# Performance work log

Hardware: AMD Instinct MI355X
Metric: run time of the kernel (lower is better)

## Reference

```python
import jax, jax.numpy as jnp
import numpy as np

# Module hyperparameters (from init_kwargs)
IOU_T = 0.5
PROB_T = 0.75
COV = 10.0
TOPK = 500       # self.topk
PRE_K = 2048     # fixed-shape cap on post-threshold candidates entering NMS
B, C, H, W = 4, 4, 160, 160


def setup_inputs() -> dict:
    key = jax.random.key(0)
    k1, k2 = jax.random.split(key)
    mask = jax.random.normal(k1, (B, C, H, W), dtype=jnp.float32)
    # scale bias so boxes have ~10px extent (realistic detections)
    bias = jax.random.normal(k2, (B, 4, H, W), dtype=jnp.float32) * 8.0
    return {"mask": mask, "bias": bias}


def _pos_grid(h, w):
    # equivalent of np.dstack(np.mgrid[0:h, 0:w]) -> [h, w, 2] with (y, x)
    yy, xx = jnp.meshgrid(jnp.arange(h), jnp.arange(w), indexing="ij")
    return jnp.stack([yy, xx], axis=-1).astype(jnp.float32)


def _pairwise_iou(b):
    # b: [K, 4] as (y1, x1, y2, x2); torchvision-style IoU (areas unclamped, inter clamped)
    area = (b[:, 2] - b[:, 0]) * (b[:, 3] - b[:, 1])
    lt = jnp.maximum(b[:, None, :2], b[None, :, :2])
    rb = jnp.minimum(b[:, None, 2:], b[None, :, 2:])
    wh = jnp.clip(rb - lt, 0.0)
    inter = wh[..., 0] * wh[..., 1]
    return inter / (area[:, None] + area[None, :] - inter)


def _nms_keep(iou, valid, thresh):
    # boxes are pre-sorted by descending score; greedy suppression
    K = iou.shape[0]
    idx = jnp.arange(K)
    def body(i, keep):
        sup = (iou[i] > thresh) & (idx > i) & keep[i]
        return keep & ~sup
    return jax.lax.fori_loop(0, K, body, valid)


def _per_image(mask_i, bias_i, pos):
    # mask_i: [C, h, w], bias_i: [4, h, w], pos: [h, w, 2]
    p = jax.nn.softmax(mask_i, axis=0)
    prob = jax.lax.stop_gradient(p.max(axis=0))          # prob.detach()
    cls = p.argmax(axis=0)
    frontal = (cls != 0) & (prob > PROB_T)               # [h, w]
    # boxes = pos tiled to (y,x,y,x) + bias.permute(0,2,3,1)
    boxes = jnp.concatenate([pos, pos], axis=-1) + jnp.transpose(bias_i, (1, 2, 0))
    boxes = boxes.reshape(-1, 4)                          # [h*w, 4]
    score = jnp.where(frontal.reshape(-1), prob.reshape(-1), -1.0)
    # fixed-size candidate set, sorted by descending score (invalid -> -1)
    top_s, idx = jax.lax.top_k(score, PRE_K)
    cand = boxes[idx]
    valid = top_s > 0.0                                   # valid scores > PROB_T > 0
    keep = _nms_keep(_pairwise_iou(cand), valid, IOU_T)
    kept_s = jnp.where(keep, top_s, -1.0)
    fin_s, fi = jax.lax.top_k(kept_s, TOPK)               # min(topk, n) via padding
    fboxes = cand[fi]                                     # [TOPK, 4]
    fvalid = fin_s > 0.0
    fprob = jnp.where(fvalid, fin_s, 0.0)
    mu = (fboxes[:, :2] + fboxes[:, 2:]) * 0.5            # [TOPK, 2]
    sigma = fboxes[:, 2:] - fboxes[:, :2]
    sigma = jnp.where(fvalid[:, None], sigma, 1.0)        # safe divisor for padding
    # gaussian2d: z = (pos - mu) / (sigma / cov); heat = max_n exp(-|z|^2/2) * prob
    z = (pos[None] - mu[:, None, None, :]) / (sigma[:, None, None, :] / COV)  # [TOPK,h,w,2]
    g = jnp.exp(-0.5 * (z ** 2).sum(axis=-1)) * fprob[:, None, None]
    heat = g.max(axis=0)                                  # [h, w]; all-padded -> 0, matches n==0 case
    return heat, fboxes, fvalid


def reference(mask, bias):
    pos = _pos_grid(mask.shape[2], mask.shape[3])
    heat, fboxes, fvalid = jax.vmap(lambda m, b: _per_image(m, b, pos))(mask, bias)
    # original returns (heatmaps, mask, boxes); boxes padded to [B, TOPK, 4] with validity mask
    return heat, mask, fboxes, fvalid
```

## Files before the change

kernel.cpp:

```cpp
#include <hip/hip_runtime.h>
#include <math.h>

#define BATCH 4
#define NCH 4
#define H 160
#define W 160
#define NPIX (H * W)
#define NTILE (NPIX / 256)
#define PRE_K 2048
#define TOPK 500
#define PROB_T 0.75f
#define IOU_T 0.5f
#define COV 10.0f

#define SCORE_OFF 0u
#define KEY_OFF   409600u
#define F_OFF     1228800u
#define CSC_OFF   1261632u
#define CBOX_OFF  1294400u
#define SUP_OFF   1425472u
#define NV_OFF    3523648u
#define PAR_OFF   3523712u
#define FLAG_OFF  3563712u
#define BCNT_OFF  3571904u

#define OUT_HEAT_OFF 0
#define OUT_MASK_OFF 102400
#define OUT_BOX_OFF  512000
#define OUT_VAL_OFF  520000

typedef unsigned long long u64;
typedef unsigned int u32;

__device__ __forceinline__ int block_scan_excl(int v, int tid, int* tmp, int* total) {
    tmp[tid] = v;
    __syncthreads();
    for (int off = 1; off < 256; off <<= 1) {
        int y = (tid >= off) ? tmp[tid - off] : 0;
        __syncthreads();
        tmp[tid] += y;
        __syncthreads();
    }
    int incl = tmp[tid];
    *total = tmp[255];
    __syncthreads();
    return incl - v;
}

__global__ void k_score(const float* __restrict__ mask, float* __restrict__ score,
                        float* __restrict__ out_mask, int* __restrict__ blkcnt) {
    int b = blockIdx.y;
    int pix = blockIdx.x * 256 + threadIdx.x;
    const float* mp = mask + (size_t)b * NCH * NPIX + pix;
    float* op = out_mask + (size_t)b * NCH * NPIX + pix;
    float x0 = mp[0], x1 = mp[NPIX], x2 = mp[2 * NPIX], x3 = mp[3 * NPIX];
    op[0] = x0; op[NPIX] = x1; op[2 * NPIX] = x2; op[3 * NPIX] = x3;
    float m = x0; int c = 0;
    if (x1 > m) { m = x1; c = 1; }
    if (x2 > m) { m = x2; c = 2; }
    if (x3 > m) { m = x3; c = 3; }
    float sum = ((expf(x0 - m) + expf(x1 - m)) + expf(x2 - m)) + expf(x3 - m);
    float prob = 1.0f / sum;
    bool frontal = (c != 0) && (prob > PROB_T);
    score[(size_t)b * NPIX + pix] = frontal ? prob : -1.0f;
    __shared__ int wcnt[4];
    u64 bm = __ballot(frontal);
    if ((threadIdx.x & 63) == 0) wcnt[threadIdx.x >> 6] = __popcll(bm);
    __syncthreads();
    if (threadIdx.x == 0)
        blkcnt[b * NTILE + blockIdx.x] = wcnt[0] + wcnt[1] + wcnt[2] + wcnt[3];
}

__global__ void __launch_bounds__(256)
k_compact(const float* __restrict__ score, const float* __restrict__ bias,
          const int* __restrict__ blkcnt, u64* __restrict__ keys,
          int* __restrict__ Fout, float* __restrict__ cand_score,
          float* __restrict__ cand_box) {
    int b = blockIdx.y;
    int bx = blockIdx.x;
    int tid = threadIdx.x;
    const int* bc = blkcnt + b * NTILE;
    int f_base = 0, F = 0;
    #pragma unroll 4
    for (int k = 0; k < NTILE; ++k) {
        int c = bc[k];
        F += c;
        if (k < bx) f_base += c;
    }
    int pix = bx * 256 + tid;
    float s = score[(size_t)b * NPIX + pix];
    bool fr = (s > 0.0f);
    int lane = tid & 63, wv = tid >> 6;
    int v = fr ? 1 : 0;
    int incl = v;
    for (int off = 1; off < 64; off <<= 1) {
        int y = __shfl_up(incl, off);
        if (lane >= off) incl += y;
    }
    __shared__ int wtot[4];
    __shared__ int wpre[4];
    if (lane == 63) wtot[wv] = incl;
    __syncthreads();
    if (tid == 0) {
        int acc = 0;
        for (int k = 0; k < 4; ++k) { wpre[k] = acc; acc += wtot[k]; }
    }
    __syncthreads();
    int f_local = wpre[wv] + (incl - v);
    if (fr) {
        u32 lo = 0x7FFFFFFFu - (u32)pix;
        keys[(size_t)b * NPIX + f_base + f_local] =
            ((u64)__float_as_uint(s) << 32) | (u64)lo;
    }
    if (bx == 0 && tid == 0) Fout[b] = F;
    if (!fr) {
        int nf_base = bx * 256 - f_base;
        int nf_local = tid - f_local;
        int slot = F + nf_base + nf_local;
        if (slot < PRE_K) {
            const float* bb = bias + (size_t)b * 4 * NPIX;
            cand_score[(size_t)b * PRE_K + slot] = -1.0f;
            float y = (float)(pix / W), x = (float)(pix % W);
            float4 box;
            box.x = y + bb[0 * NPIX + pix];
            box.y = x + bb[1 * NPIX + pix];
            box.z = y + bb[2 * NPIX + pix];
            box.w = x + bb[3 * NPIX + pix];
            ((float4*)cand_box)[(size_t)b * PRE_K + slot] = box;
        }
    }
}

#define RK_CH 4096
__global__ void k_rank(const u64* __restrict__ keys, const float* __restrict__ bias,
                       const int* __restrict__ Fout, float* __restrict__ cand_score,
                       float* __restrict__ cand_box) {
    int b = blockIdx.y;
    int F = Fout[b];
    if (blockIdx.x * 256 >= F) return;
    int i = blockIdx.x * 256 + threadIdx.x;
    const u64* kb = keys + (size_t)b * NPIX;
    u64 ki = (i < F) ? kb[i] : 0;
    int rank = 0;
    __shared__ u64 ks[RK_CH];
    for (int base = 0; base < F; base += RK_CH) {
        int lim = min(RK_CH, F - base);
        __syncthreads();
        for (int k = threadIdx.x; k < lim; k += 256) ks[k] = kb[base + k];
        __syncthreads();
        if (i < F) {
            int k = 0;
            for (; k + 8 <= lim; k += 8) {
                rank += (ks[k]     > ki) ? 1 : 0;
                rank += (ks[k + 1] > ki) ? 1 : 0;
                rank += (ks[k + 2] > ki) ? 1 : 0;
                rank += (ks[k + 3] > ki) ? 1 : 0;
                rank += (ks[k + 4] > ki) ? 1 : 0;
                rank += (ks[k + 5] > ki) ? 1 : 0;
                rank += (ks[k + 6] > ki) ? 1 : 0;
                rank += (ks[k + 7] > ki) ? 1 : 0;
            }
            for (; k < lim; ++k) rank += (ks[k] > ki) ? 1 : 0;
        }
    }
    if (i < F && rank < PRE_K) {
        float si = __uint_as_float((u32)(ki >> 32));
        int xi = 0x7FFFFFFF - (int)(u32)(ki & 0xFFFFFFFFu);
        cand_score[(size_t)b * PRE_K + rank] = si;
        const float* bb = bias + (size_t)b * 4 * NPIX;
        float y = (float)(xi / W), x = (float)(xi % W);
        float4 box;
        box.x = y + bb[0 * NPIX + xi];
        box.y = x + bb[1 * NPIX + xi];
        box.z = y + bb[2 * NPIX + xi];
        box.w = x + bb[3 * NPIX + xi];
        ((float4*)cand_box)[(size_t)b * PRE_K + rank] = box;
    }
}

__global__ void __launch_bounds__(512)
k_iou(const float* __restrict__ cand_box, const int* __restrict__ Fout,
      u32* __restrict__ sup, unsigned char* __restrict__ flag) {
    int b = blockIdx.y;
    int F = Fout[b];
    int V = F < PRE_K ? F : PRE_K;
    int r0 = blockIdx.x * 8;
    if (r0 >= V) return;
    __shared__ float ly1[PRE_K], lx1[PRE_K], ly2[PRE_K], lx2[PRE_K], lar[PRE_K];
    for (int k = threadIdx.x; k < PRE_K; k += 512) {
        float4 v = ((const float4*)cand_box)[(size_t)b * PRE_K + k];
        ly1[k] = v.x; lx1[k] = v.y; ly2[k] = v.z; lx2[k] = v.w;
        lar[k] = (v.z - v.x) * (v.w - v.y);
    }
    __syncthreads();
    int lr = threadIdx.x >> 6;
    int w = threadIdx.x & 63;
    int i = r0 + lr;
    float ay1 = ly1[i], ax1 = lx1[i], ay2 = ly2[i], ax2 = lx2[i], aa = lar[i];
    u32 bits = 0;
    int jbase = w * 32;
    #pragma unroll 4
    for (int jj = 0; jj < 32; ++jj) {
        int jo = (jj + w) & 31;
        int j = jbase + jo;
        if (j > i) {
            float lty = fmaxf(ay1, ly1[j]);
            float ltx = fmaxf(ax1, lx1[j]);
            float rby = fminf(ay2, ly2[j]);
            float rbx = fminf(ax2, lx2[j]);
            float wy = fmaxf(rby - lty, 0.0f);
            float wx = fmaxf(rbx - ltx, 0.0f);
            float inter = wy * wx;
            float iou = inter / ((aa + lar[j]) - inter);
            if (iou > IOU_T) bits |= (1u << jo);
        }
    }
    sup[((size_t)b * PRE_K + i) * 64 + w] = bits;
    bool any = __any(bits != 0u);
    if (w == 0) flag[(size_t)b * PRE_K + i] = any ? 1 : 0;
}

__global__ void __launch_bounds__(256)
k_nmsfin(const u32* __restrict__ sup, const unsigned char* __restrict__ flag,
         const int* __restrict__ Fout, const float* __restrict__ cand_score,
         const float* __restrict__ cand_box, float* __restrict__ out_boxes,
         float* __restrict__ out_valid, float* __restrict__ params,
         int* __restrict__ NV) {
    int b = blockIdx.x;
    int tid = threadIdx.x;
    int F = Fout[b];
    int V = F < PRE_K ? F : PRE_K;
    __shared__ int rid_s[PRE_K];
    __shared__ int M_s;
    __shared__ u32 kws[64];
    __shared__ int tmp[256];

    if (tid < 64) {
        int lane = tid;
        const u32* f32 = (const u32*)(flag + (size_t)b * PRE_K);
        u32 fw[8];
        #pragma unroll
        for (int k = 0; k < 8; ++k) fw[k] = f32[lane * 8 + k];
        int r0 = lane * 32;
        int cnt = 0;
        #pragma unroll
        for (int k = 0; k < 8; ++k)
            #pragma unroll
            for (int j = 0; j < 4; ++j) {
                int r = r0 + k * 4 + j;
                if (((fw[k] >> (8 * j)) & 0xFFu) != 0u && r < V) ++cnt;
            }
        int incl = cnt;
        for (int off = 1; off < 64; off <<= 1) {
            int y = __shfl_up(incl, off);
            if (lane >= off) incl += y;
        }
        if (lane == 63) M_s = incl;
        int pos = incl - cnt;
        #pragma unroll
        for (int k = 0; k < 8; ++k)
            #pragma unroll
            for (int j = 0; j < 4; ++j) {
                int r = r0 + k * 4 + j;
                if (((fw[k] >> (8 * j)) & 0xFFu) != 0u && r < V) rid_s[pos++] = r;
            }
    }
    __syncthreads();

    if (tid < 64) {
        int lane = tid;
        int M = M_s;
        int rem = V - lane * 32;
        u32 kw = (rem >= 32) ? 0xFFFFFFFFu : (rem <= 0 ? 0u : ((1u << rem) - 1u));
        const u32* supb = sup + (size_t)b * PRE_K * 64 + lane;
        int C = (M + 7) >> 3;
        int C4 = (C + 3) & ~3;
        int l7 = lane & 7;
        u32 rbuf[4][8];
        int ridv[4];

        #define LOAD_RID(slot, c) ridv[slot] = rid_s[min((c) * 8 + l7, PRE_K - 1)]
        #define ISSUE(slot) do { \
            _Pragma("unroll") \
            for (int k_ = 0; k_ < 8; ++k_) { \
                int i_ = __builtin_amdgcn_readlane(ridv[slot], k_) & (PRE_K - 1); \
                rbuf[slot][k_] = supb[(size_t)i_ * 64]; \
            } \
        } while (0)
        #define PROC(slot, c) do { \
            _Pragma("unroll") \
            for (int k_ = 0; k_ < 8; ++k_) { \
                int m_ = (c) * 8 + k_; \
                if (m_ < M) { \
                    int i_ = __builtin_amdgcn_readlane(ridv[slot], k_) & (PRE_K - 1); \
                    u32 kb_ = (u32)__builtin_amdgcn_readlane((int)kw, i_ >> 5); \
                    if ((kb_ >> (i_ & 31)) & 1u) kw &= ~rbuf[slot][k_]; \
                } \
            } \
        } while (0)

        LOAD_RID(0, 0); LOAD_RID(1, 1); LOAD_RID(2, 2); LOAD_RID(3, 3);
        ISSUE(0); ISSUE(1); ISSUE(2);
        for (int c = 0; c < C4; c += 4) {
            PROC(0, c);     ISSUE(3);            LOAD_RID(0, c + 4);
            PROC(1, c + 1); ISSUE(0);            LOAD_RID(1, c + 5);
            PROC(2, c + 2); ISSUE(1);            LOAD_RID(2, c + 6);
            PROC(3, c + 3); ISSUE(2);            LOAD_RID(3, c + 7);
        }
        #undef LOAD_RID
        #undef ISSUE
        #undef PROC
        kws[lane] = kw;
    }
    __syncthreads();

    int s0 = tid * 8;
    int bits8 = (int)((kws[s0 >> 5] >> (s0 & 31)) & 0xFFu);
    int cnt = __popc(bits8);
    int tot;
    int kpre = block_scan_excl(cnt, tid, tmp, &tot);
    int NK = tot;
    for (int k = 0; k < 8; ++k) {
        int s = s0 + k;
        int kept = (bits8 >> k) & 1;
        int pos = kept ? kpre : (NK + s - kpre);
        if (pos < TOPK) {
            float4 bx = ((const float4*)cand_box)[(size_t)b * PRE_K + s];
            ((float4*)out_boxes)[(size_t)b * TOPK + pos] = bx;
            out_valid[(size_t)b * TOPK + pos] = kept ? 1.0f : 0.0f;
            if (kept) {
                float scv = cand_score[(size_t)b * PRE_K + s];
                float* pp = params + ((size_t)b * TOPK + pos) * 5;
                pp[0] = (bx.x + bx.z) * 0.5f;
                pp[1] = (bx.y + bx.w) * 0.5f;
                pp[2] = (bx.z - bx.x) / COV;
                pp[3] = (bx.w - bx.y) / COV;
                pp[4] = scv;
            }
        }
        kpre += kept;
    }
    if (tid == 0) NV[b] = NK < TOPK ? NK : TOPK;
}

#define TILE 16
#define TPL (W / TILE)
__global__ void k_heat(const float* __restrict__ params, const int* __restrict__ NV,
                       float* __restrict__ heat) {
    int b = blockIdx.y;
    int ty0 = (blockIdx.x / TPL) * TILE;
    int tx0 = (blockIdx.x % TPL) * TILE;
    int tid = threadIdx.x;
    int nv = NV[b];
    __shared__ float lp[TOPK * 5];
    __shared__ int cntS;
    if (tid == 0) cntS = 0;
    __syncthreads();
    for (int t = tid; t < nv; t += 256) {
        const float* pp = params + ((size_t)b * TOPK + t) * 5;
        float muy = pp[0], mux = pp[1], dy = pp[2], dx = pp[3], p = pp[4];
        float cy = fmaxf(fmaxf((float)ty0 - muy, muy - (float)(ty0 + TILE - 1)), 0.0f);
        float cx = fmaxf(fmaxf((float)tx0 - mux, mux - (float)(tx0 + TILE - 1)), 0.0f);
        float zy = cy / fabsf(dy);
        float zx = cx / fabsf(dx);
        float z2 = zy * zy + zx * zx;
        if (!(z2 > 40.0f)) {
            int idx = atomicAdd(&cntS, 1);
            float* q = lp + idx * 5;
            q[0] = muy; q[1] = mux; q[2] = dy; q[3] = dx; q[4] = p;
        }
    }
    __syncthreads();
    int n = cntS;
    float py = (float)(ty0 + (tid >> 4));
    float px = (float)(tx0 + (tid & 15));
    float m = 0.0f;
    for (int t = 0; t < n; ++t) {
        float muy = lp[t * 5 + 0], mux = lp[t * 5 + 1];
        float dy = lp[t * 5 + 2], dx = lp[t * 5 + 3], p = lp[t * 5 + 4];
        float zy = (py - muy) / dy;
        float zx = (px - mux) / dx;
        float g = expf(-0.5f * (zy * zy + zx * zx)) * p;
        m = fmaxf(m, g);
    }
    heat[(size_t)b * NPIX + (ty0 + (tid >> 4)) * W + tx0 + (tid & 15)] = m;
}

extern "C" void kernel_launch(void* const* d_in, const int* in_sizes, int n_in,
                              void* d_out, int out_size, void* d_ws, size_t ws_size,
                              hipStream_t stream) {
    const float* mask = (const float*)d_in[0];
    const float* bias = (const float*)d_in[1];
    float* out = (float*)d_out;
    char* ws = (char*)d_ws;

    float* score      = (float*)(ws + SCORE_OFF);
    u64*   keys       = (u64*)(ws + KEY_OFF);
    int*   Fout       = (int*)(ws + F_OFF);
    float* cand_score = (float*)(ws + CSC_OFF);
    float* cand_box   = (float*)(ws + CBOX_OFF);
    u32*   sup        = (u32*)(ws + SUP_OFF);
    int*   NV         = (int*)(ws + NV_OFF);
    float* params     = (float*)(ws + PAR_OFF);
    unsigned char* flag = (unsigned char*)(ws + FLAG_OFF);
    int*   blkcnt     = (int*)(ws + BCNT_OFF);

    dim3 g100(NTILE, BATCH);
    k_score<<<g100, 256, 0, stream>>>(mask, score, out + OUT_MASK_OFF, blkcnt);
    k_compact<<<g100, 256, 0, stream>>>(score, bias, blkcnt, keys, Fout,
                                        cand_score, cand_box);
    k_rank<<<g100, 256, 0, stream>>>(keys, bias, Fout, cand_score, cand_box);
    k_iou<<<dim3(PRE_K / 8, BATCH), 512, 0, stream>>>(cand_box, Fout, sup, flag);
    k_nmsfin<<<BATCH, 256, 0, stream>>>(sup, flag, Fout, cand_score, cand_box,
                                        out + OUT_BOX_OFF, out + OUT_VAL_OFF, params, NV);
    k_heat<<<dim3(TPL * (H / TILE), BATCH), 256, 0, stream>>>(params, NV, out + OUT_HEAT_OFF);
}
```

Before: 115.0 us.

## Fuse compaction into scoring and NMS into heatmap, cutting kernel launches

Scoring now compacts frontal pixels directly using an atomic per-image counter and per-wave ballot masks, which removes the separate score buffer and compact kernel. Non-frontal padding slots are filled in the rank kernel by decoding the ballot masks. The NMS finalisation is redundantly recomputed in every heatmap tile block so that params never go through global memory, and the Gaussian divisions become multiplications by precomputed inverses. The suppression bitmask is only written for nonzero rows. This cuts launches and global round trips, at the cost of repeating the serial NMS work across 400 blocks, and the atomic slot order is nondeterministic but is resolved by the rank sort.

Measured after the change: 111.8 us, median of 2. -2.8%, faster.

```diff
diff --git a/kernel.cpp b/kernel.cpp
--- a/kernel.cpp
+++ b/kernel.cpp
@@ -12,22 +12,24 @@
 #define PROB_T 0.75f
 #define IOU_T 0.5f
 #define COV 10.0f
-
-#define SCORE_OFF 0u
-#define KEY_OFF   409600u
-#define F_OFF     1228800u
-#define CSC_OFF   1261632u
-#define CBOX_OFF  1294400u
-#define SUP_OFF   1425472u
-#define NV_OFF    3523648u
-#define PAR_OFF   3523712u
-#define FLAG_OFF  3563712u
-#define BCNT_OFF  3571904u
+#define RK_CH 4096
+
+#define FCNT_OFF  0u
+#define BCNT_OFF  64u
+#define BMASK_OFF 4096u
+#define KEY_OFF   20480u
+#define CSC_OFF   839680u
+#define CBOX_OFF  872448u
+#define SUP_OFF   1003520u
+#define FLAG_OFF  3100672u
 
 #define OUT_HEAT_OFF 0
 #define OUT_MASK_OFF 102400
 #define OUT_BOX_OFF  512000
 #define OUT_VAL_OFF  520000
+
+#define TILE 16
+#define TPL (W / TILE)
 
 typedef unsigned long long u64;
 typedef unsigned int u32;
@@ -47,142 +49,138 @@
     return incl - v;
 }
 
-__global__ void k_score(const float* __restrict__ mask, float* __restrict__ score,
-                        float* __restrict__ out_mask, int* __restrict__ blkcnt) {
-    int b = blockIdx.y;
-    int pix = blockIdx.x * 256 + threadIdx.x;
+__global__ void __launch_bounds__(256)
+k_score(const float* __restrict__ mask, float* __restrict__ out_mask,
+        u64* __restrict__ keys, u64* __restrict__ bmask,
+        int* __restrict__ blkcnt, int* __restrict__ Fcnt) {
+    int b = blockIdx.y, bx = blockIdx.x, tid = threadIdx.x;
+    int pix = bx * 256 + tid;
     const float* mp = mask + (size_t)b * NCH * NPIX + pix;
     float* op = out_mask + (size_t)b * NCH * NPIX + pix;
     float x0 = mp[0], x1 = mp[NPIX], x2 = mp[2 * NPIX], x3 = mp[3 * NPIX];
     op[0] = x0; op[NPIX] = x1; op[2 * NPIX] = x2; op[3 * NPIX] = x3;
-    float m = x0; int c = 0;
-    if (x1 > m) { m = x1; c = 1; }
-    if (x2 > m) { m = x2; c = 2; }
-    if (x3 > m) { m = x3; c = 3; }
-    float sum = ((expf(x0 - m) + expf(x1 - m)) + expf(x2 - m)) + expf(x3 - m);
+    float mx = x0; int c = 0;
+    if (x1 > mx) { mx = x1; c = 1; }
+    if (x2 > mx) { mx = x2; c = 2; }
+    if (x3 > mx) { mx = x3; c = 3; }
+    float sum = ((expf(x0 - mx) + expf(x1 - mx)) + expf(x2 - mx)) + expf(x3 - mx);
     float prob = 1.0f / sum;
-    bool frontal = (c != 0) && (prob > PROB_T);
-    score[(size_t)b * NPIX + pix] = frontal ? prob : -1.0f;
+    bool fr = (c != 0) && (prob > PROB_T);
+
+    int lane = tid & 63, wv = tid >> 6;
+    u64 bm = __ballot(fr);
     __shared__ int wcnt[4];
-    u64 bm = __ballot(frontal);
-    if ((threadIdx.x & 63) == 0) wcnt[threadIdx.x >> 6] = __popcll(bm);
-    __syncthreads();
-    if (threadIdx.x == 0)
-        blkcnt[b * NTILE + blockIdx.x] = wcnt[0] + wcnt[1] + wcnt[2] + wcnt[3];
-}
-
-__global__ void __launch_bounds__(256)
-k_compact(const float* __restrict__ score, const float* __restrict__ bias,
-          const int* __restrict__ blkcnt, u64* __restrict__ keys,
-          int* __restrict__ Fout, float* __restrict__ cand_score,
-          float* __restrict__ cand_box) {
-    int b = blockIdx.y;
-    int bx = blockIdx.x;
-    int tid = threadIdx.x;
-    const int* bc = blkcnt + b * NTILE;
-    int f_base = 0, F = 0;
-    #pragma unroll 4
-    for (int k = 0; k < NTILE; ++k) {
-        int c = bc[k];
-        F += c;
-        if (k < bx) f_base += c;
-    }
-    int pix = bx * 256 + tid;
-    float s = score[(size_t)b * NPIX + pix];
-    bool fr = (s > 0.0f);
-    int lane = tid & 63, wv = tid >> 6;
-    int v = fr ? 1 : 0;
-    int incl = v;
-    for (int off = 1; off < 64; off <<= 1) {
-        int y = __shfl_up(incl, off);
-        if (lane >= off) incl += y;
-    }
-    __shared__ int wtot[4];
     __shared__ int wpre[4];
-    if (lane == 63) wtot[wv] = incl;
+    __shared__ int base_s;
+    if (lane == 0) {
+        bmask[(size_t)b * (NPIX / 64) + bx * 4 + wv] = bm;
+        wcnt[wv] = __popcll(bm);
+    }
     __syncthreads();
     if (tid == 0) {
         int acc = 0;
-        for (int k = 0; k < 4; ++k) { wpre[k] = acc; acc += wtot[k]; }
-    }
-    __syncthreads();
-    int f_local = wpre[wv] + (incl - v);
+        #pragma unroll
+        for (int k = 0; k < 4; ++k) { wpre[k] = acc; acc += wcnt[k]; }
+        blkcnt[b * NTILE + bx] = acc;
+        base_s = (acc > 0) ? atomicAdd(&Fcnt[b], acc) : 0;
+    }
+    __syncthreads();
     if (fr) {
-        u32 lo = 0x7FFFFFFFu - (u32)pix;
-        keys[(size_t)b * NPIX + f_base + f_local] =
-            ((u64)__float_as_uint(s) << 32) | (u64)lo;
-    }
-    if (bx == 0 && tid == 0) Fout[b] = F;
-    if (!fr) {
-        int nf_base = bx * 256 - f_base;
-        int nf_local = tid - f_local;
-        int slot = F + nf_base + nf_local;
-        if (slot < PRE_K) {
-            const float* bb = bias + (size_t)b * 4 * NPIX;
-            cand_score[(size_t)b * PRE_K + slot] = -1.0f;
-            float y = (float)(pix / W), x = (float)(pix % W);
+        int slot = base_s + wpre[wv] + __popcll(bm & ((1ull << lane) - 1ull));
+        keys[(size_t)b * NPIX + slot] =
+            ((u64)__float_as_uint(prob) << 32) | (u64)(0x7FFFFFFFu - (u32)pix);
+    }
+}
+
+__global__ void __launch_bounds__(256)
+k_rank(const u64* __restrict__ keys, const float* __restrict__ bias,
+       const int* __restrict__ Fcnt, const int* __restrict__ blkcnt,
+       const u64* __restrict__ bmask, float* __restrict__ cand_score,
+       float* __restrict__ cand_box) {
+    int b = blockIdx.y, bx = blockIdx.x, tid = threadIdx.x;
+    int F = Fcnt[b];
+    int blk0 = bx * 256;
+    if (blk0 >= F && blk0 >= PRE_K) return;
+    int i = blk0 + tid;
+    const float* bb = bias + (size_t)b * 4 * NPIX;
+
+    __shared__ u64 ks[RK_CH];
+    if (blk0 < F) {
+        const u64* kb = keys + (size_t)b * NPIX;
+        u64 ki = (i < F) ? kb[i] : 0;
+        int rank = 0;
+        for (int base = 0; base < F; base += RK_CH) {
+            int lim = min(RK_CH, F - base);
+            __syncthreads();
+            for (int k = tid; k < lim; k += 256) ks[k] = kb[base + k];
+            __syncthreads();
+            if (i < F) {
+                int k = 0;
+                for (; k + 8 <= lim; k += 8) {
+                    rank += (ks[k]     > ki) ? 1 : 0;
+                    rank += (ks[k + 1] > ki) ? 1 : 0;
+                    rank += (ks[k + 2] > ki) ? 1 : 0;
+                    rank += (ks[k + 3] > ki) ? 1 : 0;
+                    rank += (ks[k + 4] > ki) ? 1 : 0;
+                    rank += (ks[k + 5] > ki) ? 1 : 0;
+                    rank += (ks[k + 6] > ki) ? 1 : 0;
+                    rank += (ks[k + 7] > ki) ? 1 : 0;
+                }
+                for (; k < lim; ++k) rank += (ks[k] > ki) ? 1 : 0;
+            }
+        }
+        if (i < F && rank < PRE_K) {
+            float si = __uint_as_float((u32)(ki >> 32));
+            int xi = 0x7FFFFFFF - (int)(u32)(ki & 0xFFFFFFFFu);
+            cand_score[(size_t)b * PRE_K + rank] = si;
+            float y = (float)(xi / W), x = (float)(xi % W);
             float4 box;
-            box.x = y + bb[0 * NPIX + pix];
-            box.y = x + bb[1 * NPIX + pix];
-            box.z = y + bb[2 * NPIX + pix];
-            box.w = x + bb[3 * NPIX + pix];
-            ((float4*)cand_box)[(size_t)b * PRE_K + slot] = box;
-        }
-    }
-}
-
-#define RK_CH 4096
-__global__ void k_rank(const u64* __restrict__ keys, const float* __restrict__ bias,
-                       const int* __restrict__ Fout, float* __restrict__ cand_score,
-                       float* __restrict__ cand_box) {
-    int b = blockIdx.y;
-    int F = Fout[b];
-    if (blockIdx.x * 256 >= F) return;
-    int i = blockIdx.x * 256 + threadIdx.x;
-    const u64* kb = keys + (size_t)b * NPIX;
-    u64 ki = (i < F) ? kb[i] : 0;
-    int rank = 0;
-    __shared__ u64 ks[RK_CH];
-    for (int base = 0; base < F; base += RK_CH) {
-        int lim = min(RK_CH, F - base);
-        __syncthreads();
-        for (int k = threadIdx.x; k < lim; k += 256) ks[k] = kb[base + k];
-        __syncthreads();
-        if (i < F) {
-            int k = 0;
-            for (; k + 8 <= lim; k += 8) {
-                rank += (ks[k]     > ki) ? 1 : 0;
-                rank += (ks[k + 1] > ki) ? 1 : 0;
-                rank += (ks[k + 2] > ki) ? 1 : 0;
-                rank += (ks[k + 3] > ki) ? 1 : 0;
-                rank += (ks[k + 4] > ki) ? 1 : 0;
-                rank += (ks[k + 5] > ki) ? 1 : 0;
-                rank += (ks[k + 6] > ki) ? 1 : 0;
-                rank += (ks[k + 7] > ki) ? 1 : 0;
+            box.x = y + bb[0 * NPIX + xi];
+            box.y = x + bb[1 * NPIX + xi];
+            box.z = y + bb[2 * NPIX + xi];
+            box.w = x + bb[3 * NPIX + xi];
+            ((float4*)cand_box)[(size_t)b * PRE_K + rank] = box;
+        }
+    }
+    if (i >= F && i < PRE_K) {
+        int j = i - F;
+        const int* bc = blkcnt + b * NTILE;
+        int t = 0;
+        for (; t < NTILE; ++t) {
+            int nf = 256 - bc[t];
+            if (j < nf) break;
+            j -= nf;
+        }
+        const u64* bmk = bmask + (size_t)b * (NPIX / 64) + t * 4;
+        int pix = 0;
+        #pragma unroll
+        for (int w = 0; w < 4; ++w) {
+            u64 bm = bmk[w];
+            int nz = 64 - __popcll(bm);
+            if (j < nz) {
+                u64 x = bm;
+                for (int q = 0; q < j; ++q) x |= x + 1;
+                pix = t * 256 + w * 64 + __builtin_ctzll(~x);
+                break;
             }
-            for (; k < lim; ++k) rank += (ks[k] > ki) ? 1 : 0;
-        }
-    }
-    if (i < F && rank < PRE_K) {
-        float si = __uint_as_float((u32)(ki >> 32));
-        int xi = 0x7FFFFFFF - (int)(u32)(ki & 0xFFFFFFFFu);
-        cand_score[(size_t)b * PRE_K + rank] = si;
-        const float* bb = bias + (size_t)b * 4 * NPIX;
-        float y = (float)(xi / W), x = (float)(xi % W);
+            j -= nz;
+        }
+        cand_score[(size_t)b * PRE_K + i] = -1.0f;
+        float y = (float)(pix / W), x = (float)(pix % W);
         float4 box;
-        box.x = y + bb[0 * NPIX + xi];
-        box.y = x + bb[1 * NPIX + xi];
-        box.z = y + bb[2 * NPIX + xi];
-        box.w = x + bb[3 * NPIX + xi];
-        ((float4*)cand_box)[(size_t)b * PRE_K + rank] = box;
+        box.x = y + bb[0 * NPIX + pix];
+        box.y = x + bb[1 * NPIX + pix];
+        box.z = y + bb[2 * NPIX + pix];
+        box.w = x + bb[3 * NPIX + pix];
+        ((float4*)cand_box)[(size_t)b * PRE_K + i] = box;
     }
 }
 
 __global__ void __launch_bounds__(512)
-k_iou(const float* __restrict__ cand_box, const int* __restrict__ Fout,
+k_iou(const float* __restrict__ cand_box, const int* __restrict__ Fcnt,
       u32* __restrict__ sup, unsigned char* __restrict__ flag) {
     int b = blockIdx.y;
-    int F = Fout[b];
+    int F = Fcnt[b];
     int V = F < PRE_K ? F : PRE_K;
     int r0 = blockIdx.x * 8;
     if (r0 >= V) return;
@@ -215,32 +213,34 @@
             if (iou > IOU_T) bits |= (1u << jo);
         }
     }
-    sup[((size_t)b * PRE_K + i) * 64 + w] = bits;
     bool any = __any(bits != 0u);
+    if (any) sup[((size_t)b * PRE_K + i) * 64 + w] = bits;
     if (w == 0) flag[(size_t)b * PRE_K + i] = any ? 1 : 0;
 }
 
 __global__ void __launch_bounds__(256)
-k_nmsfin(const u32* __restrict__ sup, const unsigned char* __restrict__ flag,
-         const int* __restrict__ Fout, const float* __restrict__ cand_score,
-         const float* __restrict__ cand_box, float* __restrict__ out_boxes,
-         float* __restrict__ out_valid, float* __restrict__ params,
-         int* __restrict__ NV) {
-    int b = blockIdx.x;
-    int tid = threadIdx.x;
-    int F = Fout[b];
+k_nmsheat(const u32* __restrict__ sup, const unsigned char* __restrict__ flag,
+          const int* __restrict__ Fcnt, const float* __restrict__ cand_score,
+          const float* __restrict__ cand_box, float* __restrict__ out_boxes,
+          float* __restrict__ out_valid, float* __restrict__ heat) {
+    int b = blockIdx.y, bx = blockIdx.x, tid = threadIdx.x;
+    int F = Fcnt[b];
     int V = F < PRE_K ? F : PRE_K;
+
     __shared__ int rid_s[PRE_K];
     __shared__ int M_s;
     __shared__ u32 kws[64];
     __shared__ int tmp[256];
+    __shared__ float plocal[TOPK * 5];
+    __shared__ float lp[TOPK * 5];
+    __shared__ int cnum;
 
     if (tid < 64) {
         int lane = tid;
-        const u32* f32 = (const u32*)(flag + (size_t)b * PRE_K);
+        const u32* f32p = (const u32*)(flag + (size_t)b * PRE_K);
         u32 fw[8];
         #pragma unroll
-        for (int k = 0; k < 8; ++k) fw[k] = f32[lane * 8 + k];
+        for (int k = 0; k < 8; ++k) fw[k] = f32p[lane * 8 + k];
         int r0 = lane * 32;
         int cnt = 0;
         #pragma unroll
@@ -264,11 +264,7 @@
                 int r = r0 + k * 4 + j;
                 if (((fw[k] >> (8 * j)) & 0xFFu) != 0u && r < V) rid_s[pos++] = r;
             }
-    }
-    __syncthreads();
-
-    if (tid < 64) {
-        int lane = tid;
+
         int M = M_s;
         int rem = V - lane * 32;
         u32 kw = (rem >= 32) ? 0xFFFFFFFFu : (rem <= 0 ? 0u : ((1u << rem) - 1u));
@@ -312,8 +308,10 @@
         #undef PROC
         kws[lane] = kw;
     }
-    __syncthreads();
-
+    if (tid == 0) cnum = 0;
+    __syncthreads();
+
+    bool writer = (bx == 0);
     int s0 = tid * 8;
     int bits8 = (int)((kws[s0 >> 5] >> (s0 & 31)) & 0xFFu);
     int cnt = __popc(bits8);
@@ -325,61 +323,57 @@
         int kept = (bits8 >> k) & 1;
         int pos = kept ? kpre : (NK + s - kpre);
         if (pos < TOPK) {
-            float4 bx = ((const float4*)cand_box)[(size_t)b * PRE_K + s];
-            ((float4*)out_boxes)[(size_t)b * TOPK + pos] = bx;
-            out_valid[(size_t)b * TOPK + pos] = kept ? 1.0f : 0.0f;
             if (kept) {
+                float4 bb4 = ((const float4*)cand_box)[(size_t)b * PRE_K + s];
                 float scv = cand_score[(size_t)b * PRE_K + s];
-                float* pp = params + ((size_t)b * TOPK + pos) * 5;
-                pp[0] = (bx.x + bx.z) * 0.5f;
-                pp[1] = (bx.y + bx.w) * 0.5f;
-                pp[2] = (bx.z - bx.x) / COV;
-                pp[3] = (bx.w - bx.y) / COV;
-                pp[4] = scv;
+                float* q = plocal + pos * 5;
+                q[0] = (bb4.x + bb4.z) * 0.5f;
+                q[1] = (bb4.y + bb4.w) * 0.5f;
+                q[2] = COV / (bb4.z - bb4.x);
+                q[3] = COV / (bb4.w - bb4.y);
+                q[4] = scv;
+                if (writer) {
+                    ((float4*)out_boxes)[(size_t)b * TOPK + pos] = bb4;
+                    out_valid[(size_t)b * TOPK + pos] = 1.0f;
+                }
+            } else if (writer) {
+                float4 bb4 = ((const float4*)cand_box)[(size_t)b * PRE_K + s];
+                ((float4*)out_boxes)[(size_t)b * TOPK + pos] = bb4;
+                out_valid[(size_t)b * TOPK + pos] = 0.0f;
             }
         }
         kpre += kept;
     }
-    if (tid == 0) NV[b] = NK < TOPK ? NK : TOPK;
-}
-
-#define TILE 16
-#define TPL (W / TILE)
-__global__ void k_heat(const float* __restrict__ params, const int* __restrict__ NV,
-                       float* __restrict__ heat) {
-    int b = blockIdx.y;
-    int ty0 = (blockIdx.x / TPL) * TILE;
-    int tx0 = (blockIdx.x % TPL) * TILE;
-    int tid = threadIdx.x;
-    int nv = NV[b];
-    __shared__ float lp[TOPK * 5];
-    __shared__ int cntS;
-    if (tid == 0) cntS = 0;
-    __syncthreads();
+    __syncthreads();
+
+    int nv = NK < TOPK ? NK : TOPK;
+    int ty0 = (bx / TPL) * TILE;
+    int tx0 = (bx % TPL) * TILE;
     for (int t = tid; t < nv; t += 256) {
-        const float* pp = params + ((size_t)b * TOPK + t) * 5;
-        float muy = pp[0], mux = pp[1], dy = pp[2], dx = pp[3], p = pp[4];
+        const float* pp = plocal + t * 5;
+        float muy = pp[0], mux = pp[1], ivy = pp[2], ivx = pp[3], p = pp[4];
         float cy = fmaxf(fmaxf((float)ty0 - muy, muy - (float)(ty0 + TILE - 1)), 0.0f);
         float cx = fmaxf(fmaxf((float)tx0 - mux, mux - (float)(tx0 + TILE - 1)), 0.0f);
-        float zy = cy / fabsf(dy);
-        float zx = cx / fabsf(dx);
+        float zy = cy * fabsf(ivy);
+        float zx = cx * fabsf(ivx);
         float z2 = zy * zy + zx * zx;
         if (!(z2 > 40.0f)) {
-            int idx = atomicAdd(&cntS, 1);
+            int idx = atomicAdd(&cnum, 1);
             float* q = lp + idx * 5;
-            q[0] = muy; q[1] = mux; q[2] = dy; q[3] = dx; q[4] = p;
-        }
-    }
-    __syncthreads();
-    int n = cntS;
+            q[0] = muy; q[1] = mux; q[2] = ivy; q[3] = ivx; q[4] = p;
+        }
+    }
+    __syncthreads();
+    int n = cnum;
     float py = (float)(ty0 + (tid >> 4));
     float px = (float)(tx0 + (tid & 15));
     float m = 0.0f;
     for (int t = 0; t < n; ++t) {
         float muy = lp[t * 5 + 0], mux = lp[t * 5 + 1];
-        float dy = lp[t * 5 + 2], dx = lp[t * 5 + 3], p = lp[t * 5 + 4];
-        float zy = (py - muy) / dy;
-        float zx = (px - mux) / dx;
+        float ivy = lp[t * 5 + 2], ivx = lp[t * 5 + 3];
+        float p = lp[t * 5 + 4];
+        float zy = (py - muy) * ivy;
+        float zx = (px - mux) * ivx;
         float g = expf(-0.5f * (zy * zy + zx * zx)) * p;
         m = fmaxf(m, g);
     }
@@ -394,24 +388,23 @@
     float* out = (float*)d_out;
     char* ws = (char*)d_ws;
 
-    float* score      = (float*)(ws + SCORE_OFF);
+    int*   Fcnt       = (int*)(ws + FCNT_OFF);
+    int*   blkcnt     = (int*)(ws + BCNT_OFF);
+    u64*   bmask      = (u64*)(ws + BMASK_OFF);
     u64*   keys       = (u64*)(ws + KEY_OFF);
-    int*   Fout       = (int*)(ws + F_OFF);
     float* cand_score = (float*)(ws + CSC_OFF);
     float* cand_box   = (float*)(ws + CBOX_OFF);
     u32*   sup        = (u32*)(ws + SUP_OFF);
-    int*   NV         = (int*)(ws + NV_OFF);
-    float* params     = (float*)(ws + PAR_OFF);
     unsigned char* flag = (unsigned char*)(ws + FLAG_OFF);
-    int*   blkcnt     = (int*)(ws + BCNT_OFF);
-
+
+    hipMemsetAsync(Fcnt, 0, BATCH * sizeof(int), stream);
     dim3 g100(NTILE, BATCH);
-    k_score<<<g100, 256, 0, stream>>>(mask, score, out + OUT_MASK_OFF, blkcnt);
-    k_compact<<<g100, 256, 0, stream>>>(score, bias, blkcnt, keys, Fout,
-                                        cand_score, cand_box);
-    k_rank<<<g100, 256, 0, stream>>>(keys, bias, Fout, cand_score, cand_box);
-    k_iou<<<dim3(PRE_K / 8, BATCH), 512, 0, stream>>>(cand_box, Fout, sup, flag);
-    k_nmsfin<<<BATCH, 256, 0, stream>>>(sup, flag, Fout, cand_score, cand_box,
-                                        out + OUT_BOX_OFF, out + OUT_VAL_OFF, params, NV);
-    k_heat<<<dim3(TPL * (H / TILE), BATCH), 256, 0, stream>>>(params, NV, out + OUT_HEAT_OFF);
-}
+    k_score<<<g100, 256, 0, stream>>>(mask, out + OUT_MASK_OFF, keys, bmask,
+                                      blkcnt, Fcnt);
+    k_rank<<<g100, 256, 0, stream>>>(keys, bias, Fcnt, blkcnt, bmask,
+                                     cand_score, cand_box);
+    k_iou<<<dim3(PRE_K / 8, BATCH), 512, 0, stream>>>(cand_box, Fcnt, sup, flag);
+    k_nmsheat<<<g100, 256, 0, stream>>>(sup, flag, Fcnt, cand_score, cand_box,
+                                        out + OUT_BOX_OFF, out + OUT_VAL_OFF,
+                                        out + OUT_HEAT_OFF);
+}
```
